# Kernel tuning notes

Measured on AMD Instinct MI355X. Metric: run time of the kernel, lower is better.

## Reference

```python
import jax, jax.numpy as jnp
import numpy as np

D_MODEL = 512
N_HEADS = 8
HEAD_SIZE = 64


def setup_inputs() -> dict:
    key = jax.random.key(0)
    ks = jax.random.split(key, 6)
    B, T = 4, 2048
    x_q = jax.random.normal(ks[0], (B, T, D_MODEL), dtype=jnp.float32)
    s = 1.0 / np.sqrt(D_MODEL)
    # per-head q/k/v projection weights, stacked: [H, head_size, d_model]
    Wq = jax.random.normal(ks[1], (N_HEADS, HEAD_SIZE, D_MODEL), dtype=jnp.float32) * s
    Wk = jax.random.normal(ks[2], (N_HEADS, HEAD_SIZE, D_MODEL), dtype=jnp.float32) * s
    Wv = jax.random.normal(ks[3], (N_HEADS, HEAD_SIZE, D_MODEL), dtype=jnp.float32) * s
    Wp = jax.random.normal(ks[4], (D_MODEL, D_MODEL), dtype=jnp.float32) * s
    bp = jax.random.normal(ks[5], (D_MODEL,), dtype=jnp.float32) * 0.01
    return {"x_q": x_q, "Wq": Wq, "Wk": Wk, "Wv": Wv, "Wp": Wp, "bp": bp}


def reference(x_q, Wq, Wk, Wv, Wp, bp):
    B, T, C = x_q.shape  # C == d_model
    # per-head projections: [B, H, T, K]
    q = jnp.einsum('btd,hkd->bhtk', x_q, Wq)
    k = jnp.einsum('btd,hkd->bhtk', x_q, Wk)
    v = jnp.einsum('btd,hkd->bhtk', x_q, Wv)
    # NOTE: original scales by C**-0.5 with C = d_model (not head_size)
    scores = jnp.einsum('bhtk,bhsk->bhts', q, k) * (C ** -0.5)
    causal = jnp.tril(jnp.ones((T, T), dtype=bool))
    scores = jnp.where(causal, scores, -jnp.inf)
    wei = jax.nn.softmax(scores, axis=-1)  # dropout is identity in eval
    out = jnp.einsum('bhts,bhsk->bhtk', wei, v)
    # concat heads: [B, T, H*K] == [B, T, d_model]
    out = out.transpose(0, 2, 1, 3).reshape(B, T, C)
    return out @ Wp.T + bp
```

## Files before the change

kernel.cpp:

```cpp
#include <hip/hip_runtime.h>
#include <hip/hip_bf16.h>

using bf16x8 = __attribute__((ext_vector_type(8))) __bf16;
using f32x4  = __attribute__((ext_vector_type(4))) float;
using f32x16 = __attribute__((ext_vector_type(16))) float;
using i32x4  = __attribute__((ext_vector_type(4))) int;

#define MFMA_16x16x32(a, b, c) __builtin_amdgcn_mfma_f32_16x16x32_bf16((a), (b), (c), 0, 0, 0)
#define MFMA32(a, b, c)        __builtin_amdgcn_mfma_f32_32x32x16_bf16((a), (b), (c), 0, 0, 0)

#define GLOAD16(g, l)                                                         \
    __builtin_amdgcn_global_load_lds(                                         \
        (const __attribute__((address_space(1))) unsigned int*)(g),           \
        (__attribute__((address_space(3))) unsigned int*)(l), 16, 0, 0)

__device__ __forceinline__ ushort f2bf(float f) {
    return __builtin_bit_cast(ushort, (__bf16)f);
}
__device__ __forceinline__ unsigned pk_bf16(float lo, float hi) {
    unsigned r;
    asm volatile("v_cvt_pk_bf16_f32 %0, %1, %2" : "=v"(r) : "v"(lo), "v"(hi));
    return r;
}
__device__ __forceinline__ void pl32_swap(unsigned &a, unsigned &b) {
    asm volatile("v_permlane32_swap_b32 %0, %1" : "+v"(a), "+v"(b));
}

__global__ __launch_bounds__(256) void cvt_bf16(
    const float* __restrict__ in, ushort* __restrict__ out, int n)
{
    const int i = (blockIdx.x * 256 + threadIdx.x) * 8;
    if (i + 8 <= n) {
        const f32x4 a = *(const f32x4*)(in + i);
        const f32x4 b = *(const f32x4*)(in + i + 4);
        union { ushort u[8]; i32x4 w; } p;
        #pragma unroll
        for (int j = 0; j < 4; ++j) { p.u[j] = f2bf(a[j]); p.u[4 + j] = f2bf(b[j]); }
        *(i32x4*)(out + i) = p.w;
    }
}

__global__ __launch_bounds__(256) void cvt_fused(
    const float* __restrict__ x, ushort* __restrict__ xbf, int nx, int nxb,
    const float* __restrict__ w0, const float* __restrict__ w1,
    const float* __restrict__ w2, ushort* __restrict__ wbf,
    const float* __restrict__ wp, ushort* __restrict__ wpbf)
{
    const int b = (int)blockIdx.x;
    if (b < nxb) {
        const int i = (b * 256 + (int)threadIdx.x) * 8;
        if (i + 8 <= nx) {
            const f32x4 a = *(const f32x4*)(x + i);
            const f32x4 c = *(const f32x4*)(x + i + 4);
            union { ushort u[8]; i32x4 w; } p;
            #pragma unroll
            for (int j = 0; j < 4; ++j) { p.u[j] = f2bf(a[j]); p.u[4 + j] = f2bf(c[j]); }
            *(i32x4*)(xbf + i) = p.w;
        }
    } else if (b < nxb + 384) {
        const int i = ((b - nxb) * 256 + (int)threadIdx.x) * 8;
        const int w = i >> 18, off = i & 262143;
        const float* src = (w == 0) ? w0 : ((w == 1) ? w1 : w2);
        const f32x4 a = *(const f32x4*)(src + off);
        const f32x4 c = *(const f32x4*)(src + off + 4);
        union { ushort u[8]; i32x4 v; } p;
        #pragma unroll
        for (int j = 0; j < 4; ++j) { p.u[j] = f2bf(a[j]); p.u[4 + j] = f2bf(c[j]); }
        *(i32x4*)(wbf + i) = p.v;
    } else {
        const int i = ((b - nxb - 384) * 256 + (int)threadIdx.x) * 8;
        const f32x4 a = *(const f32x4*)(wp + i);
        const f32x4 c = *(const f32x4*)(wp + i + 4);
        union { ushort u[8]; i32x4 v; } p;
        #pragma unroll
        for (int j = 0; j < 4; ++j) { p.u[j] = f2bf(a[j]); p.u[4 + j] = f2bf(c[j]); }
        *(i32x4*)(wpbf + i) = p.v;
    }
}

__global__ __launch_bounds__(256) void gemm_qkv3(
    const ushort* __restrict__ A, const ushort* __restrict__ Wbf,
    float qscale, ushort* __restrict__ qb, ushort* __restrict__ kb,
    ushort* __restrict__ vb)
{
    __shared__ ushort lA[2][128][32];
    __shared__ ushort lB[2][128][32];
    const int wsel = blockIdx.y >> 2;
    const int n0 = (blockIdx.y & 3) * 128;
    const ushort* W = Wbf + wsel * 262144;
    ushort* out = (wsel == 0) ? qb : ((wsel == 1) ? kb : vb);
    const float scale = (wsel == 0) ? qscale : 1.0f;

    const int m0 = blockIdx.x * 128;
    const int tid  = threadIdx.x;
    const int lane = tid & 63;
    const int wave = tid >> 6;
    const int wr = (wave >> 1) * 64, wc = (wave & 1) * 64;
    const int frow = lane & 15;
    const int fkp  = (((lane >> 4) ^ ((lane >> 1) & 3))) * 8;

    const int srw  = lane >> 2;
    const int scol = ((lane & 3) ^ ((lane >> 3) & 3)) * 8;

    f32x4 acc[4][4] = {};
    auto stage = [&](int k0, int b) {
        #pragma unroll
        for (int i = 0; i < 2; ++i) {
            const int rb = (wave * 2 + i) * 16;
            GLOAD16(A + (size_t)(m0 + rb + srw) * 512 + k0 + scol, &lA[b][rb][0]);
            GLOAD16(W + (size_t)(n0 + rb + srw) * 512 + k0 + scol, &lB[b][rb][0]);
        }
    };

    stage(0, 0);
    for (int t = 0; t < 16; ++t) {
        const int p = t & 1;
        __syncthreads();
        if (t + 1 < 16) stage((t + 1) * 32, p ^ 1);

        bf16x8 af[4], bg[4];
        #pragma unroll
        for (int m = 0; m < 4; ++m) af[m] = *(const bf16x8*)&lA[p][wr + m * 16 + frow][fkp];
        #pragma unroll
        for (int n = 0; n < 4; ++n) bg[n] = *(const bf16x8*)&lB[p][wc + n * 16 + frow][fkp];
        #pragma unroll
        for (int m = 0; m < 4; ++m)
            #pragma unroll
            for (int n = 0; n < 4; ++n)
                acc[m][n] = MFMA_16x16x32(af[m], bg[n], acc[m][n]);
    }

    const int rbase = (lane >> 4) * 4;
    const int ccol  = lane & 15;
    if (wsel == 2) {
        #pragma unroll
        for (int m = 0; m < 4; ++m)
            #pragma unroll
            for (int n = 0; n < 4; ++n) {
                const int col = n0 + wc + n * 16 + ccol;
                const int row0 = m0 + wr + m * 16 + rbase;
                unsigned long long u = 0;
                #pragma unroll
                for (int r = 0; r < 4; ++r)
                    u |= ((unsigned long long)f2bf(acc[m][n][r])) << (16 * r);
                const size_t idx = ((size_t)((row0 >> 11) * 8 + (col >> 6)) * 64
                                    + (col & 63)) * 2048 + (row0 & 2047);
                *(unsigned long long*)(out + idx) = u;
            }
    } else {
        #pragma unroll
        for (int m = 0; m < 4; ++m)
            #pragma unroll
            for (int n = 0; n < 4; ++n) {
                const int col = n0 + wc + n * 16 + ccol;
                #pragma unroll
                for (int r = 0; r < 4; ++r) {
                    const int row = m0 + wr + m * 16 + rbase + r;
                    out[(((row >> 11) * 8 + (col >> 6)) * 2048 + (row & 2047)) * 64 + (col & 63)]
                        = f2bf(acc[m][n][r] * scale);
                }
            }
    }
}

__global__ __launch_bounds__(256) void gemm_out(
    const ushort* __restrict__ A, const ushort* __restrict__ W,
    const float* __restrict__ bias, float* __restrict__ out)
{
    __shared__ ushort lA[2][128][32];
    __shared__ ushort lB[2][128][32];
    const int m0 = blockIdx.x * 128;
    const int n0 = blockIdx.y * 128;
    const int tid  = threadIdx.x;
    const int lane = tid & 63;
    const int wave = tid >> 6;
    const int wr = (wave >> 1) * 64, wc = (wave & 1) * 64;
    const int frow = lane & 15;
    const int fkp  = (((lane >> 4) ^ ((lane >> 1) & 3))) * 8;

    const int srw  = lane >> 2;
    const int scol = ((lane & 3) ^ ((lane >> 3) & 3)) * 8;

    f32x4 acc[4][4] = {};
    auto stage = [&](int k0, int b) {
        #pragma unroll
        for (int i = 0; i < 2; ++i) {
            const int rb = (wave * 2 + i) * 16;
            const int row = m0 + rb + srw, c = k0 + scol;
            const size_t ia = (((size_t)(row >> 11) * 8 + (c >> 6)) * 2048
                               + (row & 2047)) * 64 + (c & 63);
            GLOAD16(A + ia, &lA[b][rb][0]);
            GLOAD16(W + (size_t)(n0 + rb + srw) * 512 + k0 + scol, &lB[b][rb][0]);
        }
    };

    stage(0, 0);
    for (int t = 0; t < 16; ++t) {
        const int p = t & 1;
        __syncthreads();
        if (t + 1 < 16) stage((t + 1) * 32, p ^ 1);

        bf16x8 af[4], bg[4];
        #pragma unroll
        for (int m = 0; m < 4; ++m) af[m] = *(const bf16x8*)&lA[p][wr + m * 16 + frow][fkp];
        #pragma unroll
        for (int n = 0; n < 4; ++n) bg[n] = *(const bf16x8*)&lB[p][wc + n * 16 + frow][fkp];
        #pragma unroll
        for (int m = 0; m < 4; ++m)
            #pragma unroll
            for (int n = 0; n < 4; ++n)
                acc[m][n] = MFMA_16x16x32(af[m], bg[n], acc[m][n]);
    }

    const int rbase = (lane >> 4) * 4;
    const int ccol  = lane & 15;
    #pragma unroll
    for (int m = 0; m < 4; ++m)
        #pragma unroll
        for (int n = 0; n < 4; ++n) {
            const int col = n0 + wc + n * 16 + ccol;
            const float bv = bias[col];
            #pragma unroll
            for (int r = 0; r < 4; ++r) {
                const int row = m0 + wr + m * 16 + rbase + r;
                out[row * 512 + col] = acc[m][n][r] + bv;
            }
        }
}

__global__ __launch_bounds__(256, 2) void attn_kernel(
    const ushort* __restrict__ q, const ushort* __restrict__ k,
    const ushort* __restrict__ vt, ushort* __restrict__ att)
{
    __shared__ ushort lK[2][2][64][64];
    __shared__ ushort lV[2][2][64][64];

    const int NB   = (int)(gridDim.x * gridDim.y);
    const int NH   = NB >> 4;
    const int half = NB >> 1;
    const int n    = (int)(blockIdx.y * gridDim.x + blockIdx.x);
    const int r    = (n < half) ? n : (NB - 1 - (n - half));
    const int qt0  = (15 - r / NH) * 128;
    const int bh   = r % NH;

    const ushort* Q  = q  + (size_t)bh * 2048 * 64;
    const ushort* K  = k  + (size_t)bh * 2048 * 64;
    const ushort* VT = vt + (size_t)bh * 2048 * 64;
    ushort* O = att + (size_t)bh * 2048 * 64;

    const int tid = threadIdx.x;
    const int wv  = tid >> 6;
    const int l   = tid & 63;
    const int ql  = l & 31;
    const int hi  = l >> 5;
    const int wrow0 = qt0 + wv * 32;
    const int qrow  = wrow0 + ql;
    const int wmax  = wrow0 + 31;
    const int qkey  = ql & 7;
    const float LOG2E = 1.44269504088896f;

    const int srow = tid >> 2;
    const int sg   = (tid & 3) * 2;
    const int skey = srow & 7;

    bf16x8 aq[4];
    #pragma unroll
    for (int kk = 0; kk < 4; ++kk)
        aq[kk] = *(const bf16x8*)(Q + (size_t)qrow * 64 + kk * 16 + hi * 8);

    f32x16 o0 = {}, o1 = {};
    float mrun = -30000.0f, lrun = 0.0f;
    const int nt2 = qt0 / 128 + 1;

    i32x4 kr[2][2], vr[2][2];
    auto loadG = [&](int s0) {
        #pragma unroll
        for (int hf = 0; hf < 2; ++hf) {
            const ushort* kp = K + (size_t)(s0 + hf * 64 + srow) * 64 + (tid & 3) * 16;
            kr[hf][0] = *(const i32x4*)(kp);
            kr[hf][1] = *(const i32x4*)(kp + 8);
            const ushort* vp = VT + (size_t)srow * 2048 + s0 + hf * 64 + (tid & 3) * 16;
            vr[hf][0] = *(const i32x4*)(vp);
            vr[hf][1] = *(const i32x4*)(vp + 8);
        }
    };
    auto writeL = [&](int b) {
        #pragma unroll
        for (int hf = 0; hf < 2; ++hf) {
            *(i32x4*)&lK[b][hf][srow][((sg    ) ^ skey) * 8] = kr[hf][0];
            *(i32x4*)&lK[b][hf][srow][((sg + 1) ^ skey) * 8] = kr[hf][1];
            *(i32x4*)&lV[b][hf][srow][((sg    ) ^ skey) * 8] = vr[hf][0];
            *(i32x4*)&lV[b][hf][srow][((sg + 1) ^ skey) * 8] = vr[hf][1];
        }
    };

    loadG(0);
    writeL(0);
    if (nt2 > 1) loadG(128);

    for (int T = 0; T < nt2; ++T) {
        const int p  = T & 1;
        const int s0 = T * 128;
        __syncthreads();
        if (T + 1 < nt2) writeL(p ^ 1);
        if (T + 2 < nt2) loadG(s0 + 256);

        const bool act1 = (s0 + 64 <= wmax);

        f32x16 sa0 = {}, sb0 = {}, sa1 = {}, sb1 = {};
        #pragma unroll
        for (int kk = 0; kk < 4; ++kk) {
            const bf16x8 a0 = *(const bf16x8*)&lK[p][0][ql]     [((2 * kk + hi) ^ qkey) * 8];
            const bf16x8 b0 = *(const bf16x8*)&lK[p][0][32 + ql][((2 * kk + hi) ^ qkey) * 8];
            sa0 = MFMA32(a0, aq[kk], sa0);
            sb0 = MFMA32(b0, aq[kk], sb0);
        }
        if (act1) {
            #pragma unroll
            for (int kk = 0; kk < 4; ++kk) {
                const bf16x8 a1 = *(const bf16x8*)&lK[p][1][ql]     [((2 * kk + hi) ^ qkey) * 8];
                const bf16x8 b1 = *(const bf16x8*)&lK[p][1][32 + ql][((2 * kk + hi) ^ qkey) * 8];
                sa1 = MFMA32(a1, aq[kk], sa1);
                sb1 = MFMA32(b1, aq[kk], sb1);
            }
        }

        if (s0 + 63 > wrow0) {
            #pragma unroll
            for (int rr = 0; rr < 16; ++rr) {
                const int cr = (rr & 3) + 8 * (rr >> 2) + 4 * hi;
                if (s0 + cr > qrow)      sa0[rr] = -30000.0f;
                if (s0 + 32 + cr > qrow) sb0[rr] = -30000.0f;
            }
        }
        if (act1 && (s0 + 127 > wrow0)) {
            #pragma unroll
            for (int rr = 0; rr < 16; ++rr) {
                const int cr = (rr & 3) + 8 * (rr >> 2) + 4 * hi;
                if (s0 + 64 + cr > qrow) sa1[rr] = -30000.0f;
                if (s0 + 96 + cr > qrow) sb1[rr] = -30000.0f;
            }
        }

        float tm[16];
        #pragma unroll
        for (int rr = 0; rr < 16; ++rr) tm[rr] = fmaxf(sa0[rr], sb0[rr]);
        if (act1) {
            #pragma unroll
            for (int rr = 0; rr < 16; ++rr)
                tm[rr] = fmaxf(tm[rr], fmaxf(sa1[rr], sb1[rr]));
        }
        #pragma unroll
        for (int s = 8; s > 0; s >>= 1)
            #pragma unroll
            for (int rr = 0; rr < s; ++rr) tm[rr] = fmaxf(tm[rr], tm[rr + s]);
        float pmax = fmaxf(tm[0], __shfl_xor(tm[0], 32));

        if (__any(pmax > mrun + 8.0f)) {
            const float mnew  = fmaxf(mrun, pmax);
            const float alpha = exp2f((mrun - mnew) * LOG2E);
            mrun = mnew;
            lrun *= alpha;
            #pragma unroll
            for (int rr = 0; rr < 16; ++rr) {
                const float ar = __shfl(alpha, (rr & 3) + 8 * (rr >> 2) + 4 * hi);
                o0[rr] *= ar; o1[rr] *= ar;
            }
        }

        const float mb = mrun * LOG2E;
        #pragma unroll
        for (int rr = 0; rr < 16; ++rr) {
            sa0[rr] = exp2f(fmaf(sa0[rr], LOG2E, -mb));
            sb0[rr] = exp2f(fmaf(sb0[rr], LOG2E, -mb));
        }
        if (act1) {
            #pragma unroll
            for (int rr = 0; rr < 16; ++rr) {
                sa1[rr] = exp2f(fmaf(sa1[rr], LOG2E, -mb));
                sb1[rr] = exp2f(fmaf(sb1[rr], LOG2E, -mb));
            }
        }

        float tu[16];
        #pragma unroll
        for (int rr = 0; rr < 16; ++rr) tu[rr] = sa0[rr] + sb0[rr];
        if (act1) {
            #pragma unroll
            for (int rr = 0; rr < 16; ++rr) tu[rr] += sa1[rr] + sb1[rr];
        }
        #pragma unroll
        for (int s = 8; s > 0; s >>= 1)
            #pragma unroll
            for (int rr = 0; rr < s; ++rr) tu[rr] += tu[rr + s];
        lrun += tu[0] + __shfl_xor(tu[0], 32);

        {
            unsigned paw[4][4];
            #pragma unroll
            for (int ks = 0; ks < 4; ++ks) {
                const int e = 2 * ks, f = 2 * ks + 1;
                const int ra = 4 * (e & 3), rb = 4 * (f & 3);
                unsigned A0, A1, B0, B1;
                if (e >> 2) { A0 = pk_bf16(sb0[ra], sb0[ra + 1]); A1 = pk_bf16(sb0[ra + 2], sb0[ra + 3]); }
                else        { A0 = pk_bf16(sa0[ra], sa0[ra + 1]); A1 = pk_bf16(sa0[ra + 2], sa0[ra + 3]); }
                if (f >> 2) { B0 = pk_bf16(sb0[rb], sb0[rb + 1]); B1 = pk_bf16(sb0[rb + 2], sb0[rb + 3]); }
                else        { B0 = pk_bf16(sa0[rb], sa0[rb + 1]); B1 = pk_bf16(sa0[rb + 2], sa0[rb + 3]); }
                pl32_swap(A0, B0);
                pl32_swap(A1, B1);
                paw[ks][0] = A0; paw[ks][1] = A1; paw[ks][2] = B0; paw[ks][3] = B1;
            }
            #pragma unroll
            for (int ks = 0; ks < 4; ++ks) {
                union { unsigned w[4]; bf16x8 v; } u;
                u.w[0] = paw[ks][0]; u.w[1] = paw[ks][1];
                u.w[2] = paw[ks][2]; u.w[3] = paw[ks][3];
                const bf16x8 v0 = *(const bf16x8*)&lV[p][0][ql]     [((2 * ks + hi) ^ qkey) * 8];
                const bf16x8 v1 = *(const bf16x8*)&lV[p][0][32 + ql][((2 * ks + hi) ^ qkey) * 8];
                o0 = MFMA32(u.v, v0, o0);
                o1 = MFMA32(u.v, v1, o1);
            }
        }
        if (act1) {
            unsigned paw[4][4];
            #pragma unroll
            for (int ks = 0; ks < 4; ++ks) {
                const int e = 2 * ks, f = 2 * ks + 1;
                const int ra = 4 * (e & 3), rb = 4 * (f & 3);
                unsigned A0, A1, B0, B1;
                if (e >> 2) { A0 = pk_bf16(sb1[ra], sb1[ra + 1]); A1 = pk_bf16(sb1[ra + 2], sb1[ra + 3]); }
                else        { A0 = pk_bf16(sa1[ra], sa1[ra + 1]); A1 = pk_bf16(sa1[ra + 2], sa1[ra + 3]); }
                if (f >> 2) { B0 = pk_bf16(sb1[rb], sb1[rb + 1]); B1 = pk_bf16(sb1[rb + 2], sb1[rb + 3]); }
                else        { B0 = pk_bf16(sa1[rb], sa1[rb + 1]); B1 = pk_bf16(sa1[rb + 2], sa1[rb + 3]); }
                pl32_swap(A0, B0);
                pl32_swap(A1, B1);
                paw[ks][0] = A0; paw[ks][1] = A1; paw[ks][2] = B0; paw[ks][3] = B1;
            }
            #pragma unroll
            for (int ks = 0; ks < 4; ++ks) {
                union { unsigned w[4]; bf16x8 v; } u;
                u.w[0] = paw[ks][0]; u.w[1] = paw[ks][1];
                u.w[2] = paw[ks][2]; u.w[3] = paw[ks][3];
                const bf16x8 v0 = *(const bf16x8*)&lV[p][1][ql]     [((2 * ks + hi) ^ qkey) * 8];
                const bf16x8 v1 = *(const bf16x8*)&lV[p][1][32 + ql][((2 * ks + hi) ^ qkey) * 8];
                o0 = MFMA32(u.v, v0, o0);
                o1 = MFMA32(u.v, v1, o1);
            }
        }
    }

    const float linv = 1.0f / fmaxf(lrun, 1e-30f);
    #pragma unroll
    for (int rr = 0; rr < 16; ++rr) {
        const int cr = (rr & 3) + 8 * (rr >> 2) + 4 * hi;
        const float li = __shfl(linv, cr);
        const int row = wrow0 + cr;
        O[(size_t)row * 64 + ql]      = f2bf(o0[rr] * li);
        O[(size_t)row * 64 + 32 + ql] = f2bf(o1[rr] * li);
    }
}

extern "C" void kernel_launch(void* const* d_in, const int* in_sizes, int n_in,
                              void* d_out, int out_size, void* d_ws, size_t ws_size,
                              hipStream_t stream) {
    const float* x  = (const float*)d_in[0];
    const float* Wq = (const float*)d_in[1];
    const float* Wk = (const float*)d_in[2];
    const float* Wv = (const float*)d_in[3];
    const float* Wp = (const float*)d_in[4];
    const float* bp = (const float*)d_in[5];
    float* out = (float*)d_out;

    const size_t NEL  = 4u * 8u * 2048u * 64u;
    const size_t NELB = 8u * 2048u * 64u;
    const size_t WPN  = 262144u;
    const float qscale = 0.04419417382415922f;

    if (ws_size >= 3u * NEL * sizeof(ushort)) {
        ushort* xbf = (ushort*)d_out;
        ushort* qb  = xbf + NEL;
        ushort* kb  = (ushort*)d_ws;
        ushort* vb  = kb + NEL;
        ushort* ab  = vb + NEL;
        ushort* wbf = ab;
        const int nxb = (int)(NEL / (256 * 8));

        const bool fuse_wp = ws_size >= (3u * NEL + WPN) * sizeof(ushort);
        if (fuse_wp) {
            ushort* wpbf = ab + NEL;
            hipLaunchKernelGGL(cvt_fused, dim3(nxb + 384 + 128), dim3(256), 0, stream,
                               x, xbf, (int)NEL, nxb, Wq, Wk, Wv, wbf, Wp, wpbf);
            hipLaunchKernelGGL(gemm_qkv3, dim3(64, 12), dim3(256), 0, stream,
                               xbf, wbf, qscale, qb, kb, vb);
            hipLaunchKernelGGL(attn_kernel, dim3(16, 32), dim3(256), 0, stream, qb, kb, vb, ab);
            hipLaunchKernelGGL(gemm_out, dim3(64, 4), dim3(256), 0, stream, ab, wpbf, bp, out);
        } else {
            ushort* wpbf = kb;
            hipLaunchKernelGGL(cvt_fused, dim3(nxb + 384), dim3(256), 0, stream,
                               x, xbf, (int)NEL, nxb, Wq, Wk, Wv, wbf, Wp, wpbf);
            hipLaunchKernelGGL(gemm_qkv3, dim3(64, 12), dim3(256), 0, stream,
                               xbf, wbf, qscale, qb, kb, vb);
            hipLaunchKernelGGL(attn_kernel, dim3(16, 32), dim3(256), 0, stream, qb, kb, vb, ab);
            hipLaunchKernelGGL(cvt_bf16, dim3(128), dim3(256), 0, stream, Wp, wpbf, (int)WPN);
            hipLaunchKernelGGL(gemm_out, dim3(64, 4), dim3(256), 0, stream, ab, wpbf, bp, out);
        }
    } else {
        ushort* kb  = (ushort*)d_ws;
        ushort* vb  = kb + NELB;
        ushort* ab  = vb + NELB;
        ushort* wbf = ab;
        for (int b = 0; b < 4; ++b) {
            const float* xb = x + (size_t)b * 2048u * 512u;
            float* ob = out + (size_t)b * 2048u * 512u;
            ushort* xbf  = (ushort*)ob;
            ushort* qb   = xbf + NELB;
            ushort* wpbf = kb;
            hipLaunchKernelGGL(cvt_fused, dim3((int)(NELB / (256 * 8)) + 384), dim3(256), 0, stream,
                               xb, xbf, (int)NELB, (int)(NELB / (256 * 8)), Wq, Wk, Wv, wbf,
                               Wp, wpbf);
            hipLaunchKernelGGL(gemm_qkv3, dim3(16, 12), dim3(256), 0, stream,
                               xbf, wbf, qscale, qb, kb, vb);
            hipLaunchKernelGGL(attn_kernel, dim3(16, 8), dim3(256), 0, stream, qb, kb, vb, ab);
            hipLaunchKernelGGL(cvt_bf16, dim3(128), dim3(256), 0, stream, Wp, wpbf, (int)WPN);
            hipLaunchKernelGGL(gemm_out, dim3(16, 4), dim3(256), 0, stream, ab, wpbf, bp, ob);
        }
    }
}
```

Before: 92.88 us.

## Split long causal attention tiles into KV chunks with separate merge kernel

The attention kernel now walks a constant work table, so each of the six longest query tiles (10–15) is split into two key/value ranges processed by separate blocks. Partial outputs plus running max and sum are written to scratch, and a new merge kernel combines them with log-sum-exp weights. This is meant to even out per-block work under the causal mask and shorten the tail of the attention grid. In exchange it adds an extra launch, scratch traffic, and a bf16 rounding of the partial outputs before the merge.

```diff
diff --git a/kernel.cpp b/kernel.cpp
--- a/kernel.cpp
+++ b/kernel.cpp
@@ -17,6 +17,9 @@
 __device__ __forceinline__ ushort f2bf(float f) {
     return __builtin_bit_cast(ushort, (__bf16)f);
 }
+__device__ __forceinline__ float bf2f(ushort u) {
+    union { unsigned int i; float f; } x; x.i = ((unsigned int)u) << 16; return x.f;
+}
 __device__ __forceinline__ unsigned pk_bf16(float lo, float hi) {
     unsigned r;
     asm volatile("v_cvt_pk_bf16_f32 %0, %1, %2" : "=v"(r) : "v"(lo), "v"(hi));
@@ -25,6 +28,14 @@
 __device__ __forceinline__ void pl32_swap(unsigned &a, unsigned &b) {
     asm volatile("v_permlane32_swap_b32 %0, %1" : "+v"(a), "+v"(b));
 }
+
+#define ENC(t, a, b) ((t) | ((a) << 8) | ((b) << 16))
+__device__ __constant__ unsigned UT[22] = {
+    ENC(9,0,10), ENC(8,0,9),  ENC(15,0,8), ENC(15,8,16), ENC(14,0,8), ENC(7,0,8),
+    ENC(14,8,15),ENC(13,0,7), ENC(13,7,14),ENC(12,0,7),  ENC(6,0,7),
+    ENC(12,7,13),ENC(11,0,6), ENC(11,6,12),ENC(10,0,6),  ENC(5,0,6),
+    ENC(10,6,11),ENC(4,0,5),  ENC(3,0,4),  ENC(2,0,3),   ENC(1,0,2),  ENC(0,0,1)
+};
 
 __global__ __launch_bounds__(256) void cvt_bf16(
     const float* __restrict__ in, ushort* __restrict__ out, int n)
@@ -230,18 +241,21 @@
 
 __global__ __launch_bounds__(256, 2) void attn_kernel(
     const ushort* __restrict__ q, const ushort* __restrict__ k,
-    const ushort* __restrict__ vt, ushort* __restrict__ att)
+    const ushort* __restrict__ vt, ushort* __restrict__ att,
+    ushort* __restrict__ Ob, float* __restrict__ Mb, float* __restrict__ Lb)
 {
     __shared__ ushort lK[2][2][64][64];
     __shared__ ushort lV[2][2][64][64];
 
-    const int NB   = (int)(gridDim.x * gridDim.y);
-    const int NH   = NB >> 4;
-    const int half = NB >> 1;
-    const int n    = (int)(blockIdx.y * gridDim.x + blockIdx.x);
-    const int r    = (n < half) ? n : (NB - 1 - (n - half));
-    const int qt0  = (15 - r / NH) * 128;
-    const int bh   = r % NH;
+    const int NH   = (int)gridDim.x / 22;
+    const int n    = (int)blockIdx.x;
+    const int unit = n / NH;
+    const int bh   = n % NH;
+    const unsigned ue = UT[unit];
+    const int tile = (int)(ue & 0xff);
+    const int c0   = (int)((ue >> 8) & 0xff);
+    const int c1   = (int)((ue >> 16) & 0xff);
+    const int qt0  = tile * 128;
 
     const ushort* Q  = q  + (size_t)bh * 2048 * 64;
     const ushort* K  = k  + (size_t)bh * 2048 * 64;
@@ -270,7 +284,6 @@
 
     f32x16 o0 = {}, o1 = {};
     float mrun = -30000.0f, lrun = 0.0f;
-    const int nt2 = qt0 / 128 + 1;
 
     i32x4 kr[2][2], vr[2][2];
     auto loadG = [&](int s0) {
@@ -294,16 +307,16 @@
         }
     };
 
-    loadG(0);
-    writeL(0);
-    if (nt2 > 1) loadG(128);
-
-    for (int T = 0; T < nt2; ++T) {
+    loadG(c0 * 128);
+    writeL(c0 & 1);
+    if (c0 + 1 < c1) loadG((c0 + 1) * 128);
+
+    for (int T = c0; T < c1; ++T) {
         const int p  = T & 1;
         const int s0 = T * 128;
         __syncthreads();
-        if (T + 1 < nt2) writeL(p ^ 1);
-        if (T + 2 < nt2) loadG(s0 + 256);
+        if (T + 1 < c1) writeL(p ^ 1);
+        if (T + 2 < c1) loadG(s0 + 256);
 
         const bool act1 = (s0 + 64 <= wmax);
 
@@ -450,14 +463,61 @@
     }
 
     const float linv = 1.0f / fmaxf(lrun, 1e-30f);
+    if (tile < 10) {
+        #pragma unroll
+        for (int rr = 0; rr < 16; ++rr) {
+            const int cr = (rr & 3) + 8 * (rr >> 2) + 4 * hi;
+            const float li = __shfl(linv, cr);
+            const int row = wrow0 + cr;
+            O[(size_t)row * 64 + ql]      = f2bf(o0[rr] * li);
+            O[(size_t)row * 64 + 32 + ql] = f2bf(o1[rr] * li);
+        }
+    } else {
+        const int pi    = bh * 6 + (tile - 10);
+        const int chunk = (c0 != 0) ? 1 : 0;
+        ushort* ob = Ob + (size_t)(pi * 2 + chunk) * 128 * 64 + wv * 32 * 64;
+        #pragma unroll
+        for (int rr = 0; rr < 16; ++rr) {
+            const int cr = (rr & 3) + 8 * (rr >> 2) + 4 * hi;
+            const float li = __shfl(linv, cr);
+            ob[(size_t)cr * 64 + ql]      = f2bf(o0[rr] * li);
+            ob[(size_t)cr * 64 + 32 + ql] = f2bf(o1[rr] * li);
+        }
+        if (hi == 0) {
+            const int ri = (pi * 2 + chunk) * 128 + wv * 32 + ql;
+            Mb[ri] = mrun;
+            Lb[ri] = lrun;
+        }
+    }
+}
+
+__global__ __launch_bounds__(256) void merge_part(
+    const ushort* __restrict__ Ob, const float* __restrict__ Mb,
+    const float* __restrict__ Lb, ushort* __restrict__ att)
+{
+    const int pi   = (int)blockIdx.x;
+    const int bh   = pi / 6;
+    const int tile = 10 + pi % 6;
+    const int t    = threadIdx.x;
+    const int row  = t >> 1;
+    const int ch   = (t & 1) * 32;
+    const float LOG2E = 1.44269504088896f;
+
+    const int riA = (pi * 2 + 0) * 128 + row;
+    const int riB = (pi * 2 + 1) * 128 + row;
+    const float mA = Mb[riA], lA = Lb[riA];
+    const float mB = Mb[riB], lB = Lb[riB];
+    const float M  = fmaxf(mA, mB);
+    const float wA = lA * exp2f((mA - M) * LOG2E);
+    const float wB = lB * exp2f((mB - M) * LOG2E);
+    const float inv = 1.0f / fmaxf(wA + wB, 1e-30f);
+
+    const ushort* oa = Ob + (size_t)(pi * 2 + 0) * 128 * 64 + (size_t)row * 64 + ch;
+    const ushort* obp = Ob + (size_t)(pi * 2 + 1) * 128 * 64 + (size_t)row * 64 + ch;
+    ushort* dst = att + (size_t)bh * 2048 * 64 + (size_t)(tile * 128 + row) * 64 + ch;
     #pragma unroll
-    for (int rr = 0; rr < 16; ++rr) {
-        const int cr = (rr & 3) + 8 * (rr >> 2) + 4 * hi;
-        const float li = __shfl(linv, cr);
-        const int row = wrow0 + cr;
-        O[(size_t)row * 64 + ql]      = f2bf(o0[rr] * li);
-        O[(size_t)row * 64 + 32 + ql] = f2bf(o1[rr] * li);
-    }
+    for (int j = 0; j < 32; ++j)
+        dst[j] = f2bf((wA * bf2f(oa[j]) + wB * bf2f(obp[j])) * inv);
 }
 
 extern "C" void kernel_launch(void* const* d_in, const int* in_sizes, int n_in,
@@ -485,25 +545,27 @@
         ushort* wbf = ab;
         const int nxb = (int)(NEL / (256 * 8));
 
+        ushort* Ob = xbf;
+        float*  Mb = (float*)(xbf + 192u * 2u * 128u * 64u);
+        float*  Lb = Mb + 192u * 2u * 128u;
+
         const bool fuse_wp = ws_size >= (3u * NEL + WPN) * sizeof(ushort);
+        ushort* wpbf = fuse_wp ? (ab + NEL) : kb;
         if (fuse_wp) {
-            ushort* wpbf = ab + NEL;
             hipLaunchKernelGGL(cvt_fused, dim3(nxb + 384 + 128), dim3(256), 0, stream,
                                x, xbf, (int)NEL, nxb, Wq, Wk, Wv, wbf, Wp, wpbf);
-            hipLaunchKernelGGL(gemm_qkv3, dim3(64, 12), dim3(256), 0, stream,
-                               xbf, wbf, qscale, qb, kb, vb);
-            hipLaunchKernelGGL(attn_kernel, dim3(16, 32), dim3(256), 0, stream, qb, kb, vb, ab);
-            hipLaunchKernelGGL(gemm_out, dim3(64, 4), dim3(256), 0, stream, ab, wpbf, bp, out);
         } else {
-            ushort* wpbf = kb;
             hipLaunchKernelGGL(cvt_fused, dim3(nxb + 384), dim3(256), 0, stream,
                                x, xbf, (int)NEL, nxb, Wq, Wk, Wv, wbf, Wp, wpbf);
-            hipLaunchKernelGGL(gemm_qkv3, dim3(64, 12), dim3(256), 0, stream,
-                               xbf, wbf, qscale, qb, kb, vb);
-            hipLaunchKernelGGL(attn_kernel, dim3(16, 32), dim3(256), 0, stream, qb, kb, vb, ab);
+        }
+        hipLaunchKernelGGL(gemm_qkv3, dim3(64, 12), dim3(256), 0, stream,
+                           xbf, wbf, qscale, qb, kb, vb);
+        hipLaunchKernelGGL(attn_kernel, dim3(22 * 32), dim3(256), 0, stream,
+                           qb, kb, vb, ab, Ob, Mb, Lb);
+        hipLaunchKernelGGL(merge_part, dim3(6 * 32), dim3(256), 0, stream, Ob, Mb, Lb, ab);
+        if (!fuse_wp)
             hipLaunchKernelGGL(cvt_bf16, dim3(128), dim3(256), 0, stream, Wp, wpbf, (int)WPN);
-            hipLaunchKernelGGL(gemm_out, dim3(64, 4), dim3(256), 0, stream, ab, wpbf, bp, out);
-        }
+        hipLaunchKernelGGL(gemm_out, dim3(64, 4), dim3(256), 0, stream, ab, wpbf, bp, out);
     } else {
         ushort* kb  = (ushort*)d_ws;
         ushort* vb  = kb + NELB;
@@ -515,12 +577,17 @@
             ushort* xbf  = (ushort*)ob;
             ushort* qb   = xbf + NELB;
             ushort* wpbf = kb;
+            ushort* Ob = xbf;
+            float*  Mb = (float*)(xbf + 48u * 2u * 128u * 64u);
+            float*  Lb = Mb + 48u * 2u * 128u;
             hipLaunchKernelGGL(cvt_fused, dim3((int)(NELB / (256 * 8)) + 384), dim3(256), 0, stream,
                                xb, xbf, (int)NELB, (int)(NELB / (256 * 8)), Wq, Wk, Wv, wbf,
                                Wp, wpbf);
             hipLaunchKernelGGL(gemm_qkv3, dim3(16, 12), dim3(256), 0, stream,
                                xbf, wbf, qscale, qb, kb, vb);
-            hipLaunchKernelGGL(attn_kernel, dim3(16, 8), dim3(256), 0, stream, qb, kb, vb, ab);
+            hipLaunchKernelGGL(attn_kernel, dim3(22 * 8), dim3(256), 0, stream,
+                               qb, kb, vb, ab, Ob, Mb, Lb);
+            hipLaunchKernelGGL(merge_part, dim3(6 * 8), dim3(256), 0, stream, Ob, Mb, Lb, ab);
             hipLaunchKernelGGL(cvt_bf16, dim3(128), dim3(256), 0, stream, Wp, wpbf, (int)WPN);
             hipLaunchKernelGGL(gemm_out, dim3(16, 4), dim3(256), 0, stream, ab, wpbf, bp, ob);
         }
```

Measured after the change: 92.07 us. About the same (-0.9%).
